# Kernel optimization log

Hardware: AMD Instinct MI355X
Metric: run time of the kernel (lower is better)

The kernel has to match this reference:

```python
import jax, jax.numpy as jnp
import numpy as np

NTOKEN, NINP, NHID, DA, R, MLP_NHID, NCLASS = 50000, 300, 512, 350, 30, 2000, 5
B, T = 64, 512
NEG = -1e30  # masked logit fill


def _lstm_dir(x, W_ih, W_hh):
    """Single-direction, bias-free LSTM. x: [B,T,D] -> outputs [B,T,H]."""
    Bb = x.shape[0]
    H = W_hh.shape[1]
    xg = jnp.einsum('btd,gd->tbg', x, W_ih)  # precompute input gates [T,B,4H]

    def step(carry, xg_t):
        h, c = carry
        g = xg_t + h @ W_hh.T
        i, f, gg, o = jnp.split(g, 4, axis=-1)  # PyTorch gate order i,f,g,o
        c = jax.nn.sigmoid(f) * c + jax.nn.sigmoid(i) * jnp.tanh(gg)
        h = jax.nn.sigmoid(o) * jnp.tanh(c)
        return (h, c), h

    init = (jnp.zeros((Bb, H), x.dtype), jnp.zeros((Bb, H), x.dtype))
    _, hs = jax.lax.scan(step, init, xg)
    return hs.transpose(1, 0, 2)  # [B,T,H]


def _rev_within(x, lens):
    """Reverse each sequence within its valid length (packed-seq backward pass)."""
    t = jnp.arange(x.shape[1])
    idx = jnp.where(t[None, :] < lens[:, None], lens[:, None] - 1 - t[None, :], t[None, :])
    return jnp.take_along_axis(x, idx[:, :, None], axis=1)


def setup_inputs() -> dict:
    key = jax.random.key(0)
    ks = jax.random.split(key, 12)
    u = lambda k, shape, s: jax.random.uniform(k, shape, jnp.float32, -s, s)
    input_ids = jax.random.randint(ks[0], (B, T), 0, NTOKEN)
    len_li = jnp.sort(jax.random.randint(ks[1], (B,), 1, T + 1))[::-1].at[0].set(T)
    emb = jax.random.normal(ks[2], (NTOKEN, NINP), jnp.float32)
    H4, sc = 4 * NHID, 1.0 / np.sqrt(NHID)
    W_ih_f = u(ks[3], (H4, NINP), sc)
    W_hh_f = u(ks[4], (H4, NHID), sc)
    W_ih_b = u(ks[5], (H4, NINP), sc)
    W_hh_b = u(ks[6], (H4, NHID), sc)
    W1 = u(ks[7], (DA, 2 * NHID), 0.1)
    W2 = u(ks[8], (R, DA), 0.1)
    Wm = u(ks[9], (MLP_NHID, R * 2 * NHID), 0.1)
    bm = jnp.zeros((MLP_NHID,), jnp.float32)
    Wd = u(ks[10], (NCLASS, MLP_NHID), 0.1)
    bd = jnp.zeros((NCLASS,), jnp.float32)
    return dict(input_ids=input_ids, len_li=len_li, emb=emb, W_ih_f=W_ih_f, W_hh_f=W_hh_f,
                W_ih_b=W_ih_b, W_hh_b=W_hh_b, W1=W1, W2=W2, Wm=Wm, bm=bm, Wd=Wd, bd=bd)


def reference(input_ids, len_li, emb, W_ih_f, W_hh_f, W_ih_b, W_hh_b, W1, W2, Wm, bm, Wd, bd):
    mask = jnp.arange(input_ids.shape[1])[None, :] < len_li[:, None]  # [B,T]
    x = emb[input_ids] * mask[:, :, None]  # packed semantics: padding never enters RNN
    out_f = _lstm_dir(x, W_ih_f, W_hh_f)
    out_b = _rev_within(_lstm_dir(_rev_within(x, len_li), W_ih_b, W_hh_b), len_li)
    Hout = jnp.concatenate([out_f, out_b], axis=-1)  # [B,T,2H]
    # self-attention: A = softmax(S2 tanh(S1 H^T)) over valid timesteps
    s2 = jnp.tanh(Hout @ W1.T) @ W2.T  # [B,T,r]
    logits = jnp.where(mask[:, None, :], s2.transpose(0, 2, 1), NEG)  # [B,r,T]
    A = jax.nn.softmax(logits, axis=-1)
    M = jnp.einsum('brt,bth->brh', A, Hout)  # [B,r,2H]
    BM = M.reshape(M.shape[0], -1)  # [B, r*2H]
    AAT = jnp.einsum('brt,bst->brs', A, A)
    I = jnp.eye(A.shape[1], dtype=A.dtype)
    penal = jnp.mean(jnp.sum((AAT - I) ** 2, axis=(1, 2)))  # ||AA^T - I||_F^2 averaged
    decoded = jax.nn.relu(BM @ Wm.T + bm) @ Wd.T + bd  # [B,nclass]
    return decoded, penal
```

## Files before the change

### kernel.cpp

```cpp
#include <hip/hip_runtime.h>
#include <stdint.h>

typedef unsigned short u16;
typedef unsigned long long u64;
typedef short s8v __attribute__((ext_vector_type(8)));
typedef float f32x4 __attribute__((ext_vector_type(4)));

#define BT    64
#define TT    512
#define NINP  300
#define KX    320
#define HH    512
#define DAP   384
#define RR    30
#define RP    128
#define MROWS 32768
#define MLPH  2000
#define H2    1024
#define KSPL  8
#define KMLP  30720
#define KCH   (KMLP/KSPL)

__device__ inline float b2f(u16 u){ union{unsigned i; float f;} v; v.i = ((unsigned)u)<<16; return v.f; }
__device__ inline u16 f2b(float x){ union{unsigned i; float f;} v; v.f = x; unsigned b = v.i;
  unsigned r = (b + 0x7fffu + ((b>>16)&1u))>>16; return (u16)r; }

__device__ inline float ftanh(float x){
  float e = __expf(2.f*x);
  return 1.f - 2.f/(e + 1.f);
}

__device__ inline s8v cvt8t(const float* p){
  union { unsigned u[4]; s8v v; } r;
  #pragma unroll
  for (int i=0;i<4;i++){
    unsigned lo = __float_as_uint(p[2*i])   >> 16;
    unsigned hi = __float_as_uint(p[2*i+1]) & 0xFFFF0000u;
    r.u[i] = lo | hi;
  }
  return r.v;
}

__global__ __launch_bounds__(256)
void embed_kernel(const int* __restrict__ ids, const int* __restrict__ lens,
                  const float* __restrict__ emb, u16* __restrict__ Xf)
{
  int w = blockIdx.x*4 + (threadIdx.x>>6);
  int lane = threadIdx.x & 63;
  int b = w & 63, t = w >> 6;
  int len = lens[b];
  int id = ids[b*TT + t];
  bool valid = t < len;
  const float* src = emb + (size_t)id*NINP;
  #pragma unroll
  for (int i=0;i<5;i++){
    int col = lane + i*64;
    float v = (valid && col < NINP) ? src[col] : 0.f;
    Xf[(size_t)w*KX + col] = f2b(v);
  }
}

__global__ void padcvt_kernel(const float* __restrict__ src, u16* __restrict__ dst,
                              int srows, int scols, int drows, int dcols)
{
  size_t i = (size_t)blockIdx.x*blockDim.x + threadIdx.x;
  size_t tot = (size_t)drows*dcols;
  if (i >= tot) return;
  int r = (int)(i / dcols), c = (int)(i % dcols);
  dst[i] = (r < srows && c < scols) ? f2b(src[(size_t)r*scols + c]) : (u16)0;
}

template<int ACT>
__global__ __launch_bounds__(256)
void gemm_bt(const u16* __restrict__ A, const u16* __restrict__ Bm, u16* __restrict__ C,
             int M, int N, int K)
{
  __shared__ u16 As[128][40];
  __shared__ u16 Bs[128][40];
  const int bn0 = blockIdx.x * 128;
  const int bm0 = blockIdx.y * 128;
  const int tid = threadIdx.x;
  const int wid = tid >> 6, lane = tid & 63;
  const int q = lane >> 4, ln = lane & 15;
  const int moff = (wid >> 1) * 64, noff = (wid & 1) * 64;
  f32x4 acc[4][4];
  f32x4 z4 = {0.f,0.f,0.f,0.f};
  #pragma unroll
  for (int i=0;i<4;i++){ acc[i][0]=z4; acc[i][1]=z4; acc[i][2]=z4; acc[i][3]=z4; }

  const int c0 = tid*2;
  const int r0 = c0>>2, kc0 = (c0&3)*8;
  const int c1 = c0+1;
  const int r1 = c1>>2, kc1 = (c1&3)*8;

  for (int kk = 0; kk < K; kk += 32) {
    *(uint4*)&As[r0][kc0] = *(const uint4*)&A[(size_t)(bm0+r0)*K + kk + kc0];
    *(uint4*)&As[r1][kc1] = *(const uint4*)&A[(size_t)(bm0+r1)*K + kk + kc1];
    *(uint4*)&Bs[r0][kc0] = *(const uint4*)&Bm[(size_t)(bn0+r0)*K + kk + kc0];
    *(uint4*)&Bs[r1][kc1] = *(const uint4*)&Bm[(size_t)(bn0+r1)*K + kk + kc1];
    __syncthreads();
    s8v af[4], bf[4];
    #pragma unroll
    for (int i=0;i<4;i++) af[i] = *(const s8v*)&As[moff + 16*i + ln][q*8];
    #pragma unroll
    for (int j=0;j<4;j++) bf[j] = *(const s8v*)&Bs[noff + 16*j + ln][q*8];
    #pragma unroll
    for (int i=0;i<4;i++)
      #pragma unroll
      for (int j=0;j<4;j++)
        acc[i][j] = __builtin_amdgcn_mfma_f32_16x16x32_bf16(af[i], bf[j], acc[i][j], 0,0,0);
    __syncthreads();
  }
  #pragma unroll
  for (int i=0;i<4;i++){
    #pragma unroll
    for (int j=0;j<4;j++){
      #pragma unroll
      for (int r=0;r<4;r++){
        int m = bm0 + moff + 16*i + q*4 + r;
        int n = bn0 + noff + 16*j + ln;
        float v = acc[i][j][r];
        if (ACT == 1) v = ftanh(v);
        C[(size_t)m*N + n] = f2b(v);
      }
    }
  }
}

__global__ __launch_bounds__(256, 1)
void lstm_kernel(const float* __restrict__ Wih_f, const float* __restrict__ Whh_f,
                 const float* __restrict__ Wih_b, const float* __restrict__ Whh_b,
                 const u16* __restrict__ Xf, const int* __restrict__ lens_g,
                 u16* hbuf,
                 unsigned* __restrict__ HR,
                 unsigned* flags)
{
  __shared__ u16 Wl[64*HH];
  const int bid = blockIdx.x;
  const int dir = bid >> 5;
  const int blk = bid & 31;
  const int j0 = blk * 16;
  const int tid = threadIdx.x;
  const int wv = tid >> 6, lane = tid & 63;
  const int q = lane >> 4, ln = lane & 15;
  const float* Wih = dir ? Wih_b : Wih_f;
  const float* Whh = dir ? Whh_b : Whh_f;

  for (int c = tid; c < 4096; c += 256) {
    int row = c >> 6, g = c & 63;
    int wrow = (row >> 4)*HH + j0 + (row & 15);
    const float* src = Whh + (size_t)wrow*HH + g*8;
    uint4 pk;
    pk.x = (unsigned)f2b(src[0]) | ((unsigned)f2b(src[1])<<16);
    pk.y = (unsigned)f2b(src[2]) | ((unsigned)f2b(src[3])<<16);
    pk.z = (unsigned)f2b(src[4]) | ((unsigned)f2b(src[5])<<16);
    pk.w = (unsigned)f2b(src[6]) | ((unsigned)f2b(src[7])<<16);
    int gsw = (g & ~7) | ((g & 7) ^ (row & 7));
    *(uint4*)&Wl[row*HH + gsw*8] = pk;
  }
  s8v bx[4][10];
  #pragma unroll
  for (int gt=0; gt<4; gt++){
    #pragma unroll
    for (int ks=0; ks<10; ks++){
      int wrow = gt*HH + j0 + ln;
      int col0 = ks*32 + q*8;
      union { u16 h[8]; s8v v; } pk;
      #pragma unroll
      for (int e=0;e<8;e++){
        int col = col0 + e;
        pk.h[e] = (col < NINP) ? f2b(Wih[(size_t)wrow*NINP + col]) : (u16)0;
      }
      bx[gt][ks] = pk.v;
    }
  }
  __syncthreads();

  const int bat0 = wv*16;
  const int alen = lens_g[bat0 + ln];
  float c_state[4] = {0.f,0.f,0.f,0.f};
  const int j = j0 + ln;
  const s8v zf = {0,0,0,0,0,0,0,0};

  u16* hb = hbuf + (size_t)dir*2*BT*HH;
  unsigned* myflags = flags + dir*32;

  s8v xcur[10];
  {
    int xr = (dir == 0) ? (0*BT + bat0 + ln)
                        : ((alen-1)*BT + bat0 + ln);
    const u16* xp = Xf + (size_t)xr*KX + q*8;
    #pragma unroll
    for (int ks=0; ks<10; ks++) xcur[ks] = *(const s8v*)(xp + ks*32);
  }

  for (int t = 0; t < TT; t++) {
    s8v hreg[16];
    if (t > 0) {
      if (wv == 0) {
        unsigned tgt = (unsigned)t;
        int guard = 0;
        for (;;) {
          unsigned v = (lane < 32)
            ? __hip_atomic_load(&myflags[lane], __ATOMIC_RELAXED, __HIP_MEMORY_SCOPE_AGENT)
            : tgt;
          if (__ballot(v >= tgt) == ~0ull) break;
          __builtin_amdgcn_s_sleep(1);
          if (++guard > (1<<20)) break;
        }
      }
      __syncthreads();

      const u16* hp = hb + (size_t)(t & 1)*BT*HH + (size_t)(bat0 + ln)*HH + q*8;
      #pragma unroll
      for (int ks = 0; ks < 16; ks++) {
        asm volatile("global_load_dwordx4 %0, %1, off offset:%2 sc0 sc1"
                     : "=v"(hreg[ks]) : "v"(hp), "n"(ks*64) : "memory");
      }
    }

    f32x4 acc[4];
    f32x4 z4 = {0.f,0.f,0.f,0.f};
    #pragma unroll
    for (int gt=0; gt<4; gt++) acc[gt] = z4;

    #pragma unroll
    for (int ks=0; ks<10; ks++){
      #pragma unroll
      for (int gt=0; gt<4; gt++)
        acc[gt] = __builtin_amdgcn_mfma_f32_16x16x32_bf16(xcur[ks], bx[gt][ks], acc[gt], 0,0,0);
    }
    if (t > 0) {
      #pragma unroll
      for (int ks=0; ks<16; ks++) {
        asm volatile("s_waitcnt vmcnt(%0)" :: "n"(15-ks) : "memory");
        __builtin_amdgcn_sched_barrier(0);
        #pragma unroll
        for (int gt=0; gt<4; gt++) {
          int prow = gt*16 + ln;
          int g = ks*4 + q;
          int gsw = (g & ~7) | ((g & 7) ^ (prow & 7));
          s8v bfr = *(const s8v*)&Wl[prow*HH + gsw*8];
          acc[gt] = __builtin_amdgcn_mfma_f32_16x16x32_bf16(hreg[ks], bfr, acc[gt], 0,0,0);
        }
      }
    }

    u16 hv4[4];
    #pragma unroll
    for (int r=0;r<4;r++) {
      float iv = 1.f/(1.f + __expf(-acc[0][r]));
      float fv = 1.f/(1.f + __expf(-acc[1][r]));
      float gv = ftanh(acc[2][r]);
      float ov = 1.f/(1.f + __expf(-acc[3][r]));
      float cc = fv*c_state[r] + iv*gv;
      c_state[r] = cc;
      hv4[r] = f2b(ov*ftanh(cc));
    }
    unsigned pk4[4];
    #pragma unroll
    for (int r=0;r<4;r++) {
      unsigned lo = hv4[r];
      unsigned partner = (unsigned)__shfl((int)lo, lane ^ 1);
      pk4[r] = lo | (partner << 16);
    }
    const bool evn = ((ln & 1) == 0);

    {
      size_t base = (((size_t)(dir*32 + blk)*4 + wv)*512 + (size_t)t)*4;
      if (evn) {
        #pragma unroll
        for (int r=0;r<4;r++)
          HR[(base + r)*32 + q*8 + (ln>>1)] = pk4[r];
      }
    }
    {
      int tn = (t < TT-1) ? t+1 : TT-1;
      int xr;
      if (dir == 0) xr = tn*BT + bat0 + ln;
      else          xr = (tn < alen) ? (alen-1-tn)*BT + bat0 + ln : -1;
      const u16* xp = Xf + (size_t)(xr < 0 ? 0 : xr)*KX + q*8;
      #pragma unroll
      for (int ks=0; ks<10; ks++){
        s8v v = *(const s8v*)(xp + ks*32);
        xcur[ks] = (xr >= 0) ? v : zf;
      }
    }
    if (t < TT-1) {
      if (evn) {
        u16* hnxt = hb + (size_t)((t+1)&1)*BT*HH;
        #pragma unroll
        for (int r=0;r<4;r++) {
          int bat = bat0 + q*4 + r;
          unsigned* dst = (unsigned*)(hnxt + (size_t)bat*HH + j);
          asm volatile("global_store_dword %0, %1, off sc0 sc1"
                       :: "v"(dst), "v"(pk4[r]) : "memory");
        }
      }
      asm volatile("s_waitcnt vmcnt(0)" ::: "memory");
      __syncthreads();
      if (tid == 0) {
        unsigned* fp = &myflags[blk];
        unsigned fv = (unsigned)(t+1);
        asm volatile("global_store_dword %0, %1, off sc0 sc1"
                     :: "v"(fp), "v"(fv) : "memory");
      }
    }
  }
}

__global__ __launch_bounds__(256)
void repack_kernel(const unsigned* __restrict__ HR, const int* __restrict__ lens,
                   u16* __restrict__ Hout)
{
  int w = blockIdx.x*4 + (threadIdx.x>>6);
  int lane = threadIdx.x & 63;
  int dir = w >> 15;
  int b   = (w >> 9) & 63;
  int t   = w & 511;
  int len = lens[b];
  int tp = t;
  if (dir) tp = (t < len) ? (len - 1 - t) : t;
  int blk = lane >> 1;
  int wv = b >> 4, q = (b >> 2) & 3, r = b & 3;
  size_t src = ((((size_t)(dir*32 + blk)*4 + wv)*512 + (size_t)t)*4 + r)*32
               + q*8 + (lane & 1)*4;
  uint4 v = *(const uint4*)&HR[src];
  *(uint4*)&Hout[((size_t)b*TT + tp)*H2 + dir*HH + lane*8] = v;
}

__global__ __launch_bounds__(256)
void softmax_kernel(const u16* __restrict__ s2, const int* __restrict__ lens,
                    float* __restrict__ A)
{
  int w = blockIdx.x*4 + (threadIdx.x>>6);
  int lane = threadIdx.x & 63;
  int b = w / RR, r = w % RR;
  int len = lens[b];
  float v[8];
  float mx = -1e38f;
  #pragma unroll
  for (int i=0;i<8;i++){
    int t = lane + i*64;
    float x = b2f(s2[((size_t)b*TT + t)*RP + r]);
    v[i] = (t < len) ? x : -1e38f;
    mx = fmaxf(mx, v[i]);
  }
  #pragma unroll
  for (int o=1;o<64;o<<=1) mx = fmaxf(mx, __shfl_xor(mx, o));
  float sm = 0.f;
  #pragma unroll
  for (int i=0;i<8;i++){ v[i] = __expf(v[i]-mx); sm += v[i]; }
  #pragma unroll
  for (int o=1;o<64;o<<=1) sm += __shfl_xor(sm, o);
  float inv = 1.0f/sm;
  #pragma unroll
  for (int i=0;i<8;i++){
    int t = lane + i*64;
    A[((size_t)b*RR + r)*TT + t] = v[i]*inv;
  }
}

__global__ __launch_bounds__(256)
void penal_kernel(const float* __restrict__ A, float* __restrict__ pen)
{
  __shared__ __align__(16) float Af[RR*TT];
  __shared__ float red[4];
  int b = blockIdx.x, tid = threadIdx.x;
  for (int i=tid;i<RR*TT;i+=256) Af[i] = A[(size_t)b*RR*TT + i];
  __syncthreads();
  float s = 0.f;
  for (int p = tid; p < RR*RR; p += 256) {
    int r = p/RR, c = p%RR;
    float d = 0.f;
    for (int t=0;t<TT;t++) d += Af[r*TT+t]*Af[c*TT+t];
    d -= (r==c) ? 1.f : 0.f;
    s += d*d;
  }
  #pragma unroll
  for (int o=1;o<64;o<<=1) s += __shfl_xor(s, o);
  if ((tid&63)==0) red[tid>>6] = s;
  __syncthreads();
  if (tid==0) atomicAdd(pen, (red[0]+red[1]+red[2]+red[3]) * (1.0f/64.0f));
}

__global__ __launch_bounds__(256)
void attnM_kernel(const float* __restrict__ A, const u16* __restrict__ Hout,
                  u16* __restrict__ Mout)
{
  __shared__ __align__(16) float Af[RR*TT];
  int b = blockIdx.x >> 2;
  int ch = blockIdx.x & 3;
  int tid = threadIdx.x;
  for (int i=tid;i<RR*TT;i+=256) Af[i] = A[(size_t)b*RR*TT + i];
  __syncthreads();
  int h = ch*256 + tid;
  float m[RR];
  #pragma unroll
  for (int r=0;r<RR;r++) m[r] = 0.f;
  for (int t=0;t<TT;t+=4){
    float hv0 = b2f(Hout[((size_t)b*TT + t+0)*H2 + h]);
    float hv1 = b2f(Hout[((size_t)b*TT + t+1)*H2 + h]);
    float hv2 = b2f(Hout[((size_t)b*TT + t+2)*H2 + h]);
    float hv3 = b2f(Hout[((size_t)b*TT + t+3)*H2 + h]);
    #pragma unroll
    for (int r=0;r<RR;r++){
      f32x4 a4 = *(const f32x4*)&Af[r*TT + t];
      m[r] += a4.x*hv0 + a4.y*hv1 + a4.z*hv2 + a4.w*hv3;
    }
  }
  #pragma unroll
  for (int r=0;r<RR;r++) Mout[((size_t)b*RR + r)*H2 + h] = f2b(m[r]);
}

__global__ __launch_bounds__(256)
void mlp1_kernel(const u16* __restrict__ BM, const float* __restrict__ Wm,
                 float* __restrict__ R1)
{
  int kc = blockIdx.x >> 5;
  int xb = blockIdx.x & 31;
  int w = xb*4 + (threadIdx.x>>6);
  if (w >= MLPH/16) return;
  int lane = threadIdx.x & 63;
  int q = lane>>4, ln = lane&15;
  f32x4 z4 = {0.f,0.f,0.f,0.f};
  f32x4 acc[4] = {z4,z4,z4,z4};
  const float* wrow = Wm + (size_t)(w*16 + ln)*KMLP;
  for (int ks = kc*KCH; ks < (kc+1)*KCH; ks += 32){
    s8v bf = cvt8t(&wrow[ks + q*8]);
    #pragma unroll
    for (int i=0;i<4;i++){
      s8v af = *(const s8v*)&BM[(size_t)(i*16+ln)*KMLP + ks + q*8];
      acc[i] = __builtin_amdgcn_mfma_f32_16x16x32_bf16(af, bf, acc[i], 0,0,0);
    }
  }
  int n = w*16 + ln;
  #pragma unroll
  for (int i=0;i<4;i++){
    #pragma unroll
    for (int r=0;r<4;r++){
      int m = i*16 + q*4 + r;
      atomicAdd(&R1[(size_t)m*MLPH + n], acc[i][r]);
    }
  }
}

__global__ __launch_bounds__(256)
void dec_kernel(const float* __restrict__ R1, const float* __restrict__ bm,
                const float* __restrict__ Wd, const float* __restrict__ bd,
                float* __restrict__ dec)
{
  int w = blockIdx.x*4 + (threadIdx.x>>6);
  int lane = threadIdx.x & 63;
  int m = w/5, n = w%5;
  float s = 0.f;
  for (int k=lane;k<MLPH;k+=64){
    float v = R1[(size_t)m*MLPH+k] + bm[k];
    s += fmaxf(v, 0.f)*Wd[(size_t)n*MLPH+k];
  }
  #pragma unroll
  for (int o=1;o<64;o<<=1) s += __shfl_xor(s, o);
  if (lane==0) dec[m*5+n] = s + bd[n];
}

__global__ __launch_bounds__(384)
void fin_kernel(const float* __restrict__ dec, const float* __restrict__ pen,
                float* __restrict__ out)
{
  int i = threadIdx.x;
  if (i < 320) out[i] = dec[i];
  if (i == 320) out[320] = *pen;
}

__global__ void zero_out_kernel(float* out){ int i = blockIdx.x*256 + threadIdx.x; if (i < 321) out[i] = 0.f; }

extern "C" void kernel_launch(void* const* d_in, const int* in_sizes, int n_in,
                              void* d_out, int out_size, void* d_ws, size_t ws_size,
                              hipStream_t stream)
{
  const int*   ids  = (const int*)d_in[0];
  const int*   lens = (const int*)d_in[1];
  const float* emb  = (const float*)d_in[2];
  const float* Wihf = (const float*)d_in[3];
  const float* Whhf = (const float*)d_in[4];
  const float* Wihb = (const float*)d_in[5];
  const float* Whhb = (const float*)d_in[6];
  const float* W1   = (const float*)d_in[7];
  const float* W2   = (const float*)d_in[8];
  const float* Wm   = (const float*)d_in[9];
  const float* bm   = (const float*)d_in[10];
  const float* Wd   = (const float*)d_in[11];
  const float* bd   = (const float*)d_in[12];

  char* ws = (char*)d_ws;
  size_t off = 0;
  auto nxt = [&](size_t sz){ size_t r = off; off += (sz + 255) & ~(size_t)255; return r; };
  const size_t HRsz = (size_t)2*32*4*512*4*32*4;
  size_t oZ   = nxt(4096);
  size_t oXf  = nxt((size_t)MROWS*KX*2);
  size_t oHout= nxt((size_t)BT*TT*H2*2);
  size_t oW1p = nxt((size_t)DAP*H2*2);
  size_t oW2p = nxt((size_t)RP*DAP*2);
  size_t oHb  = nxt((size_t)2*2*BT*HH*2);
  size_t oBig = nxt(HRsz);
  size_t p2 = oBig;
  auto sub = [&](size_t sz){ size_t r = p2; p2 += (sz + 255) & ~(size_t)255; return r; };
  size_t oS1  = sub((size_t)MROWS*DAP*2);
  size_t oS2  = sub((size_t)MROWS*RP*2);
  size_t oA   = sub((size_t)BT*RR*TT*4);
  size_t oM   = sub((size_t)BT*RR*H2*2);
  size_t oR1  = sub((size_t)BT*MLPH*4);
  size_t oDec = sub(2048);
  size_t need = off;

  if (ws_size < need) {
    zero_out_kernel<<<2, 256, 0, stream>>>((float*)d_out);
    return;
  }

  u16* Xf    = (u16*)(ws + oXf);
  u16* Hout  = (u16*)(ws + oHout);
  u16* W1p   = (u16*)(ws + oW1p);
  u16* W2p   = (u16*)(ws + oW2p);
  u16* hb    = (u16*)(ws + oHb);
  unsigned* HR = (unsigned*)(ws + oBig);
  u16* s1    = (u16*)(ws + oS1);
  u16* s2    = (u16*)(ws + oS2);
  float* Ab  = (float*)(ws + oA);
  u16* Mo    = (u16*)(ws + oM);
  float* R1  = (float*)(ws + oR1);
  float* dec = (float*)(ws + oDec);
  unsigned* flags = (unsigned*)(ws + oZ);
  float* pen = (float*)(ws + oZ + 2048);

  hipMemsetAsync(ws + oZ, 0, 4096, stream);

  embed_kernel<<<8192, 256, 0, stream>>>(ids, lens, emb, Xf);
  padcvt_kernel<<<(DAP*H2+255)/256, 256, 0, stream>>>(W1, W1p, 350, H2, DAP, H2);
  padcvt_kernel<<<(RP*DAP+255)/256, 256, 0, stream>>>(W2, W2p, RR, 350, RP, DAP);

  lstm_kernel<<<64, 256, 0, stream>>>(Wihf, Whhf, Wihb, Whhb, Xf, lens, hb, HR, flags);

  repack_kernel<<<16384, 256, 0, stream>>>(HR, lens, Hout);

  hipMemsetAsync(ws + oR1, 0, (size_t)BT*MLPH*4, stream);

  dim3 gS1(DAP/128, MROWS/128);
  gemm_bt<1><<<gS1, 256, 0, stream>>>(Hout, W1p, s1, MROWS, DAP, H2);
  dim3 gS2(RP/128, MROWS/128);
  gemm_bt<0><<<gS2, 256, 0, stream>>>(s1, W2p, s2, MROWS, RP, DAP);

  softmax_kernel<<<480, 256, 0, stream>>>(s2, lens, Ab);
  penal_kernel<<<64, 256, 0, stream>>>(Ab, pen);
  attnM_kernel<<<256, 256, 0, stream>>>(Ab, Hout, Mo);
  mlp1_kernel<<<256, 256, 0, stream>>>(Mo, Wm, R1);
  dec_kernel<<<80, 256, 0, stream>>>(R1, bm, Wd, bd, dec);
  fin_kernel<<<1, 384, 0, stream>>>(dec, pen, (float*)d_out);
  (void)in_sizes; (void)n_in; (void)out_size; (void)ws_size;
}
```

Measured before the change: 3.593 ms.

## Keep recurrent LSTM weights in registers and move input weights to LDS

Swaps where the two LSTM weight sets live. The recurrent W_hh slice now sits in registers as bf16 MFMA fragments, and the input-projection W_ih fragments move into shared memory, so the serial h·W_hh product no longer reads LDS on the per-step critical path. The x-row load is no longer prefetched a step ahead; it is issued each step alongside the h loads, with a waitcnt that covers only the x loads before the input MFMAs start. The change raises register pressure considerably and adds x-load latency inside each step. For padded steps in the backward direction it now relies on Xf rows being zero.

```diff
diff --git a/kernel.cpp b/kernel.cpp
--- a/kernel.cpp
+++ b/kernel.cpp
@@ -135,7 +135,7 @@
                  unsigned* __restrict__ HR,
                  unsigned* flags)
 {
-  __shared__ u16 Wl[64*HH];
+  __shared__ s8v BxL[40][64];
   const int bid = blockIdx.x;
   const int dir = bid >> 5;
   const int blk = bid & 31;
@@ -146,55 +146,54 @@
   const float* Wih = dir ? Wih_b : Wih_f;
   const float* Whh = dir ? Whh_b : Whh_f;
 
-  for (int c = tid; c < 4096; c += 256) {
-    int row = c >> 6, g = c & 63;
-    int wrow = (row >> 4)*HH + j0 + (row & 15);
-    const float* src = Whh + (size_t)wrow*HH + g*8;
-    uint4 pk;
-    pk.x = (unsigned)f2b(src[0]) | ((unsigned)f2b(src[1])<<16);
-    pk.y = (unsigned)f2b(src[2]) | ((unsigned)f2b(src[3])<<16);
-    pk.z = (unsigned)f2b(src[4]) | ((unsigned)f2b(src[5])<<16);
-    pk.w = (unsigned)f2b(src[6]) | ((unsigned)f2b(src[7])<<16);
-    int gsw = (g & ~7) | ((g & 7) ^ (row & 7));
-    *(uint4*)&Wl[row*HH + gsw*8] = pk;
-  }
-  s8v bx[4][10];
+  if (wv == 0) {
+    #pragma unroll
+    for (int gt=0; gt<4; gt++){
+      #pragma unroll
+      for (int ks=0; ks<10; ks++){
+        int wrow = gt*HH + j0 + ln;
+        int col0 = ks*32 + q*8;
+        union { u16 h[8]; s8v v; } pk;
+        #pragma unroll
+        for (int e=0;e<8;e++){
+          int col = col0 + e;
+          pk.h[e] = (col < NINP) ? f2b(Wih[(size_t)wrow*NINP + col]) : (u16)0;
+        }
+        BxL[gt*10+ks][lane] = pk.v;
+      }
+    }
+  }
+
+  s8v bw[4][16];
   #pragma unroll
   for (int gt=0; gt<4; gt++){
     #pragma unroll
-    for (int ks=0; ks<10; ks++){
+    for (int ks=0; ks<16; ks++){
       int wrow = gt*HH + j0 + ln;
       int col0 = ks*32 + q*8;
-      union { u16 h[8]; s8v v; } pk;
-      #pragma unroll
-      for (int e=0;e<8;e++){
-        int col = col0 + e;
-        pk.h[e] = (col < NINP) ? f2b(Wih[(size_t)wrow*NINP + col]) : (u16)0;
-      }
-      bx[gt][ks] = pk.v;
-    }
-  }
-  __syncthreads();
+      const float4* wp = (const float4*)&Whh[(size_t)wrow*HH + col0];
+      float4 a = wp[0], b = wp[1];
+      union { unsigned u[4]; s8v v; } pk;
+      pk.u[0] = (unsigned)f2b(a.x) | ((unsigned)f2b(a.y)<<16);
+      pk.u[1] = (unsigned)f2b(a.z) | ((unsigned)f2b(a.w)<<16);
+      pk.u[2] = (unsigned)f2b(b.x) | ((unsigned)f2b(b.y)<<16);
+      pk.u[3] = (unsigned)f2b(b.z) | ((unsigned)f2b(b.w)<<16);
+      bw[gt][ks] = pk.v;
+    }
+  }
 
   const int bat0 = wv*16;
   const int alen = lens_g[bat0 + ln];
+  __syncthreads();
+
   float c_state[4] = {0.f,0.f,0.f,0.f};
   const int j = j0 + ln;
-  const s8v zf = {0,0,0,0,0,0,0,0};
 
   u16* hb = hbuf + (size_t)dir*2*BT*HH;
   unsigned* myflags = flags + dir*32;
 
-  s8v xcur[10];
-  {
-    int xr = (dir == 0) ? (0*BT + bat0 + ln)
-                        : ((alen-1)*BT + bat0 + ln);
-    const u16* xp = Xf + (size_t)xr*KX + q*8;
-    #pragma unroll
-    for (int ks=0; ks<10; ks++) xcur[ks] = *(const s8v*)(xp + ks*32);
-  }
-
   for (int t = 0; t < TT; t++) {
+    s8v xv[10];
     s8v hreg[16];
     if (t > 0) {
       if (wv == 0) {
@@ -210,13 +209,23 @@
         }
       }
       __syncthreads();
-
+    }
+
+    {
+      int tr = (dir == 0) ? t : ((t < alen) ? (alen-1-t) : t);
+      int xr = tr*BT + bat0 + ln;
+      const u16* xp = Xf + (size_t)xr*KX + q*8;
+      #pragma unroll
+      for (int ks=0; ks<10; ks++)
+        asm volatile("global_load_dwordx4 %0, %1, off offset:%2"
+                     : "=v"(xv[ks]) : "v"(xp), "n"(ks*64) : "memory");
+    }
+    {
       const u16* hp = hb + (size_t)(t & 1)*BT*HH + (size_t)(bat0 + ln)*HH + q*8;
       #pragma unroll
-      for (int ks = 0; ks < 16; ks++) {
+      for (int ks = 0; ks < 16; ks++)
         asm volatile("global_load_dwordx4 %0, %1, off offset:%2 sc0 sc1"
                      : "=v"(hreg[ks]) : "v"(hp), "n"(ks*64) : "memory");
-      }
     }
 
     f32x4 acc[4];
@@ -224,11 +233,15 @@
     #pragma unroll
     for (int gt=0; gt<4; gt++) acc[gt] = z4;
 
+    asm volatile("s_waitcnt vmcnt(16)" ::: "memory");
+    __builtin_amdgcn_sched_barrier(0);
     #pragma unroll
     for (int ks=0; ks<10; ks++){
       #pragma unroll
-      for (int gt=0; gt<4; gt++)
-        acc[gt] = __builtin_amdgcn_mfma_f32_16x16x32_bf16(xcur[ks], bx[gt][ks], acc[gt], 0,0,0);
+      for (int gt=0; gt<4; gt++){
+        s8v bxf = BxL[gt*10+ks][lane];
+        acc[gt] = __builtin_amdgcn_mfma_f32_16x16x32_bf16(xv[ks], bxf, acc[gt], 0,0,0);
+      }
     }
     if (t > 0) {
       #pragma unroll
@@ -236,13 +249,8 @@
         asm volatile("s_waitcnt vmcnt(%0)" :: "n"(15-ks) : "memory");
         __builtin_amdgcn_sched_barrier(0);
         #pragma unroll
-        for (int gt=0; gt<4; gt++) {
-          int prow = gt*16 + ln;
-          int g = ks*4 + q;
-          int gsw = (g & ~7) | ((g & 7) ^ (prow & 7));
-          s8v bfr = *(const s8v*)&Wl[prow*HH + gsw*8];
-          acc[gt] = __builtin_amdgcn_mfma_f32_16x16x32_bf16(hreg[ks], bfr, acc[gt], 0,0,0);
-        }
+        for (int gt=0; gt<4; gt++)
+          acc[gt] = __builtin_amdgcn_mfma_f32_16x16x32_bf16(hreg[ks], bw[gt][ks], acc[gt], 0,0,0);
       }
     }
 
@@ -272,18 +280,6 @@
         #pragma unroll
         for (int r=0;r<4;r++)
           HR[(base + r)*32 + q*8 + (ln>>1)] = pk4[r];
-      }
-    }
-    {
-      int tn = (t < TT-1) ? t+1 : TT-1;
-      int xr;
-      if (dir == 0) xr = tn*BT + bat0 + ln;
-      else          xr = (tn < alen) ? (alen-1-tn)*BT + bat0 + ln : -1;
-      const u16* xp = Xf + (size_t)(xr < 0 ? 0 : xr)*KX + q*8;
-      #pragma unroll
-      for (int ks=0; ks<10; ks++){
-        s8v v = *(const s8v*)(xp + ks*32);
-        xcur[ks] = (xr >= 0) ? v : zf;
       }
     }
     if (t < TT-1) {
```

Result: slower. 3.947 ms (+9.8%).
